# Performance work log

Measured on AMD Instinct MI355X. Metric: run time of the kernel, lower is better.

Reference implementation:

```python
import jax, jax.numpy as jnp
import numpy as np

N_HEADS = 16
LN_EPS = 1e-6


def _mha(q_in, kv_in, mask, wq, bq, wk, bk, wv, bv, wo, bo):
    B, Sq, D = q_in.shape
    H = N_HEADS
    dh = D // H
    def split(x):  # [B,S,D] -> [B,H,S,dh]
        return x.reshape(B, -1, H, dh).transpose(0, 2, 1, 3)
    q = split(q_in @ wq + bq)
    k = split(kv_in @ wk + bk)
    v = split(kv_in @ wv + bv)
    scores = jnp.einsum('bhqd,bhkd->bhqk', q, k) / jnp.sqrt(jnp.asarray(dh, q.dtype))
    scores = scores + mask * (-1e9)
    attn = jax.nn.softmax(scores, axis=-1)
    out = jnp.einsum('bhqk,bhkd->bhqd', attn, v)
    out = out.transpose(0, 2, 1, 3).reshape(B, Sq, D)
    return out @ wo + bo


def _layer_norm(x, gamma, beta):
    mu = jnp.mean(x, axis=-1, keepdims=True)
    var = jnp.mean(jnp.square(x - mu), axis=-1, keepdims=True)
    return (x - mu) * jax.lax.rsqrt(var + LN_EPS) * gamma + beta


def setup_inputs() -> dict:
    key = jax.random.key(0)
    B, S_dec, S_enc, D, F = 4, 1024, 1024, 1024, 4096
    ks = jax.random.split(key, 16)
    s = 0.02
    inp = {
        'inputs': jax.random.normal(ks[0], (B, S_dec, D), jnp.float32),
        'enc_outputs': jax.random.normal(ks[1], (B, S_enc, D), jnp.float32),
        # causal look-ahead mask: 1 above diagonal -> -1e9 added to scores
        'mask_1': jnp.triu(jnp.ones((S_dec, S_dec), jnp.float32), k=1)[None, None],
        'mask_2': jnp.zeros((B, 1, 1, S_enc), jnp.float32),
    }
    names = ['wq1', 'wk1', 'wv1', 'wo1', 'wq2', 'wk2', 'wv2', 'wo2']
    for i, n in enumerate(names):
        inp[n] = jax.random.normal(ks[2 + i], (D, D), jnp.float32) * s
        inp['b' + n[1:]] = jnp.zeros((D,), jnp.float32)
    inp['w_ff1'] = jax.random.normal(ks[10], (D, F), jnp.float32) * s
    inp['b_ff1'] = jnp.zeros((F,), jnp.float32)
    inp['w_ff2'] = jax.random.normal(ks[11], (F, D), jnp.float32) * s
    inp['b_ff2'] = jnp.zeros((D,), jnp.float32)
    for i in (1, 2, 3):
        inp[f'g{i}'] = jnp.ones((D,), jnp.float32)
        inp[f'beta{i}'] = jnp.zeros((D,), jnp.float32)
    return inp


def reference(inputs, enc_outputs, mask_1, mask_2,
              wq1, bq1, wk1, bk1, wv1, bv1, wo1, bo1,
              wq2, bq2, wk2, bk2, wv2, bv2, wo2, bo2,
              w_ff1, b_ff1, w_ff2, b_ff2,
              g1, beta1, g2, beta2, g3, beta3):
    # causal self-attention + residual + LN (dropout inactive at inference)
    attn = _mha(inputs, inputs, mask_1, wq1, bq1, wk1, bk1, wv1, bv1, wo1, bo1)
    attn = _layer_norm(attn + inputs, g1, beta1)
    # encoder-decoder cross-attention + residual + LN
    attn2 = _mha(attn, enc_outputs, mask_2, wq2, bq2, wk2, bk2, wv2, bv2, wo2, bo2)
    attn2 = _layer_norm(attn2 + attn, g2, beta2)
    # FFN + residual + LN
    h = jax.nn.relu(attn2 @ w_ff1 + b_ff1)
    h = h @ w_ff2 + b_ff2
    return _layer_norm(h + attn2, g3, beta3)
```

## Files before the change

kernel.cpp:

```cpp
#include <hip/hip_runtime.h>
#include <stdint.h>

typedef unsigned short ushort_t;
typedef __attribute__((ext_vector_type(8))) short bf16x8;
typedef __attribute__((ext_vector_type(4))) float f32x4;
typedef __attribute__((ext_vector_type(4))) unsigned short us4;

#define DEV __device__ __forceinline__

DEV unsigned short f2bf(float f) {
  union { float f; unsigned u; } x; x.f = f;
  unsigned r = x.u + 0x7fffu + ((x.u >> 16) & 1u);
  return (unsigned short)(r >> 16);
}

DEV void gload16(const void* g, void* l) {
  __builtin_amdgcn_global_load_lds(
      (const __attribute__((address_space(1))) unsigned int*)g,
      (__attribute__((address_space(3))) unsigned int*)l, 16, 0, 0);
}

#define MFMA16 __builtin_amdgcn_mfma_f32_16x16x32_bf16

__global__ __launch_bounds__(256) void cast_bf16_kernel(
    const float* __restrict__ x, ushort_t* __restrict__ y, int n4) {
  int i = blockIdx.x * 256 + threadIdx.x;
  if (i >= n4) return;
  float4 v = ((const float4*)x)[i];
  us4 o; o.x = f2bf(v.x); o.y = f2bf(v.y); o.z = f2bf(v.z); o.w = f2bf(v.w);
  ((us4*)y)[i] = o;
}

__global__ __launch_bounds__(256) void reduce_cast_kernel(
    const float* __restrict__ p0, const float* __restrict__ p1,
    ushort_t* __restrict__ y, int n4) {
  int i = blockIdx.x * 256 + threadIdx.x;
  if (i >= n4) return;
  float4 a = ((const float4*)p0)[i];
  float4 b = ((const float4*)p1)[i];
  us4 o; o.x = f2bf(a.x + b.x); o.y = f2bf(a.y + b.y);
  o.z = f2bf(a.z + b.z); o.w = f2bf(a.w + b.w);
  ((us4*)y)[i] = o;
}

__global__ __launch_bounds__(256) void transpose_cast_kernel(
    const float* __restrict__ W, ushort_t* __restrict__ dst, int K, int N) {
  __shared__ float tile[64][65];
  int n0 = blockIdx.x * 64, k0 = blockIdx.y * 64;
  int tid = threadIdx.x;
#pragma unroll
  for (int it = 0; it < 16; ++it) {
    int idx = it * 256 + tid; int r = idx >> 6, c = idx & 63;
    tile[r][c] = W[(size_t)(k0 + r) * N + n0 + c];
  }
  __syncthreads();
#pragma unroll
  for (int it = 0; it < 16; ++it) {
    int idx = it * 256 + tid; int r = idx >> 6, c = idx & 63;
    dst[(size_t)(n0 + r) * K + k0 + c] = f2bf(tile[c][r]);
  }
}

struct Src8 { const float* p[8]; };
__global__ __launch_bounds__(256) void transpose_cast8_kernel(
    Src8 s, ushort_t* __restrict__ dst) {
  __shared__ float tile[64][65];
  const float* W = s.p[blockIdx.z];
  ushort_t* out = dst + (size_t)blockIdx.z * 1048576;
  int n0 = blockIdx.x * 64, k0 = blockIdx.y * 64;
  int tid = threadIdx.x;
#pragma unroll
  for (int it = 0; it < 16; ++it) {
    int idx = it * 256 + tid; int r = idx >> 6, c = idx & 63;
    tile[r][c] = W[(size_t)(k0 + r) * 1024 + n0 + c];
  }
  __syncthreads();
#pragma unroll
  for (int it = 0; it < 16; ++it) {
    int idx = it * 256 + tid; int r = idx >> 6, c = idx & 63;
    out[(size_t)(n0 + r) * 1024 + k0 + c] = f2bf(tile[c][r]);
  }
}

__global__ __launch_bounds__(256) void transpose_v_kernel(
    const ushort_t* __restrict__ V, int ldv, ushort_t* __restrict__ vT) {
  __shared__ ushort_t tile[64][65];
  int s0 = blockIdx.x * 64;
  int bh = blockIdx.y;
  int b = bh >> 4, h = bh & 15;
  int tid = threadIdx.x;
#pragma unroll
  for (int it = 0; it < 4; ++it) {
    int idx = it * 256 + tid; int r = idx >> 4, c = (idx & 15) * 4;
    us4 v = *(const us4*)&V[(size_t)(b * 1024 + s0 + r) * ldv + h * 64 + c];
    tile[r][c] = v.x; tile[r][c + 1] = v.y; tile[r][c + 2] = v.z; tile[r][c + 3] = v.w;
  }
  __syncthreads();
#pragma unroll
  for (int it = 0; it < 4; ++it) {
    int idx = it * 256 + tid; int r = idx >> 4, c = (idx & 15) * 4;
    us4 o; o.x = tile[c][r]; o.y = tile[c + 1][r]; o.z = tile[c + 2][r]; o.w = tile[c + 3][r];
    *(us4*)&vT[((size_t)bh * 64 + r) * 1024 + s0 + c] = o;
  }
}

template <int WF32, int WB16, int RELU>
__global__ __launch_bounds__(256, 2) void gemm_bt(
    const ushort_t* __restrict__ A, const ushort_t* __restrict__ Bt,
    const float* __restrict__ b0, const float* __restrict__ b1,
    const float* __restrict__ b2, const float* __restrict__ b3,
    float* __restrict__ Cf, ushort_t* __restrict__ Cb,
    int M, int N, int K, int Ks, long long pstr) {
  __shared__ ushort_t sA[4096];
  __shared__ ushort_t sB[4096];
  const int tid = threadIdx.x;
  const int w = tid >> 6, lane = tid & 63;
  const int lrow = lane & 15, lk = lane >> 4;
  const int m0 = blockIdx.x * 128, n0 = blockIdx.y * 128;
  const int kz = blockIdx.z * Ks;
  const int wr = w >> 1, wc = w & 1;
  f32x4 acc[4][4] = {};
  const int brow0 = (w * 1024 + lane * 16) >> 6;
  const int kbyte = (lane * 16) & 63;

  for (int kt = kz; kt < kz + Ks; kt += 32) {
    __syncthreads();
    const ushort_t* ga = A + (size_t)(m0 + brow0) * K + kt + (kbyte >> 1);
    gload16(ga, (char*)sA + w * 1024);
    gload16(ga + (size_t)64 * K, (char*)sA + 4096 + w * 1024);
    const ushort_t* gb = Bt + (size_t)(n0 + brow0) * K + kt + (kbyte >> 1);
    gload16(gb, (char*)sB + w * 1024);
    gload16(gb + (size_t)64 * K, (char*)sB + 4096 + w * 1024);
    __syncthreads();
    bf16x8 aF[4], bF[4];
#pragma unroll
    for (int t = 0; t < 4; ++t) {
      aF[t] = *(const bf16x8*)((const char*)sA + ((wr * 64 + t * 16 + lrow) << 6) + (lk << 4));
      bF[t] = *(const bf16x8*)((const char*)sB + ((wc * 64 + t * 16 + lrow) << 6) + (lk << 4));
    }
#pragma unroll
    for (int mt = 0; mt < 4; ++mt)
#pragma unroll
      for (int nt = 0; nt < 4; ++nt)
        acc[mt][nt] = MFMA16(aF[mt], bF[nt], acc[mt][nt], 0, 0, 0);
  }
  float* Cfz = Cf + (long long)blockIdx.z * pstr;
#pragma unroll
  for (int nt = 0; nt < 4; ++nt) {
    int col = n0 + wc * 64 + nt * 16 + lrow;
    int seg = col >> 10;
    const float* bp = seg == 0 ? b0 : seg == 1 ? b1 : seg == 2 ? b2 : b3;
    float bv = bp[col & 1023];
    if (blockIdx.z != 0) bv = 0.f;
#pragma unroll
    for (int mt = 0; mt < 4; ++mt) {
      int rowb = m0 + wr * 64 + mt * 16 + lk * 4;
#pragma unroll
      for (int j = 0; j < 4; ++j) {
        float v = acc[mt][nt][j] + bv;
        if (RELU) v = fmaxf(v, 0.f);
        size_t idx = (size_t)(rowb + j) * N + col;
        if (WF32) Cfz[idx] = v;
        if (WB16) Cb[idx] = f2bf(v);
      }
    }
  }
}

template <int WF32, int WB16, int RELU>
__global__ __launch_bounds__(512, 1) void gemm256(
    const ushort_t* __restrict__ A, const ushort_t* __restrict__ Bt,
    const float* __restrict__ b0, const float* __restrict__ b1,
    const float* __restrict__ b2, const float* __restrict__ b3,
    float* __restrict__ Cf, ushort_t* __restrict__ Cb,
    int M, int N, int K, int Ks, long long pstr) {
  extern __shared__ char L[];
  const int tid = threadIdx.x;
  const int w = tid >> 6, lane = tid & 63;
  const int lrow = lane & 15, lk = lane >> 4;
  const int wm = w >> 2, wn = w & 3;
  const int m0 = blockIdx.x * 256, n0 = blockIdx.y * 256;
  const int kz = blockIdx.z * Ks;
  const int nt = Ks >> 6;

  const int srow = w * 8 + (lane >> 3);
  const int gsw = (lane & 7) ^ ((lane >> 3) & 7);
  const ushort_t* srcA = A + (size_t)(m0 + srow) * K + kz + gsw * 8;
  const ushort_t* srcB = Bt + (size_t)(n0 + srow) * K + kz + gsw * 8;
  const int dstw = w * 1024;

#define STG(M_, T_)                                                   \
  do {                                                                \
    const ushort_t* g0 = ((M_) ? srcB : srcA) + (size_t)(T_) * 64;    \
    char* d_ = L + (((T_) & 1) << 16) + ((M_) << 15) + dstw;          \
    gload16(g0, d_);                                                  \
    gload16(g0 + (size_t)64 * K, d_ + 8192);                          \
    gload16(g0 + (size_t)128 * K, d_ + 16384);                        \
    gload16(g0 + (size_t)192 * K, d_ + 24576);                        \
  } while (0)

  f32x4 acc[8][4] = {};
  const int swz = (lrow & 7) << 4;
  const int k0b = (lk << 4) ^ swz;
  const int k1b = (64 + (lk << 4)) ^ swz;
  const int aBase = (wm * 128 + lrow) << 7;
  const int bBase = ((wn * 64 + lrow) << 7) + 32768;

  STG(0, 0); STG(1, 0); STG(0, 1);
  asm volatile("s_waitcnt vmcnt(4)" ::: "memory");
  __builtin_amdgcn_s_barrier();

  for (int t = 0; t < nt; ++t) {
    const int buf = (t & 1) << 16;
    const char* base = L + buf;
    bf16x8 aF[8], bF0, bF1;
    {
#pragma unroll
      for (int m = 0; m < 8; ++m) aF[m] = *(const bf16x8*)(base + aBase + m * 2048 + k0b);
      bF0 = *(const bf16x8*)(base + bBase + k0b);
      bF1 = *(const bf16x8*)(base + bBase + 2048 + k0b);
      if (t + 1 < nt) STG(1, t + 1);
      __builtin_amdgcn_s_barrier();
      __builtin_amdgcn_s_setprio(1);
#pragma unroll
      for (int m = 0; m < 8; ++m) {
        acc[m][0] = MFMA16(aF[m], bF0, acc[m][0], 0, 0, 0);
        acc[m][1] = MFMA16(aF[m], bF1, acc[m][1], 0, 0, 0);
      }
      __builtin_amdgcn_s_setprio(0);
      __builtin_amdgcn_s_barrier();
    }
    {
      bF0 = *(const bf16x8*)(base + bBase + 4096 + k0b);
      bF1 = *(const bf16x8*)(base + bBase + 6144 + k0b);
      __builtin_amdgcn_s_barrier();
      __builtin_amdgcn_s_setprio(1);
#pragma unroll
      for (int m = 0; m < 8; ++m) {
        acc[m][2] = MFMA16(aF[m], bF0, acc[m][2], 0, 0, 0);
        acc[m][3] = MFMA16(aF[m], bF1, acc[m][3], 0, 0, 0);
      }
      __builtin_amdgcn_s_setprio(0);
      __builtin_amdgcn_s_barrier();
    }
    {
#pragma unroll
      for (int m = 0; m < 8; ++m) aF[m] = *(const bf16x8*)(base + aBase + m * 2048 + k1b);
      bF0 = *(const bf16x8*)(base + bBase + k1b);
      bF1 = *(const bf16x8*)(base + bBase + 2048 + k1b);
      __builtin_amdgcn_s_barrier();
      __builtin_amdgcn_s_setprio(1);
#pragma unroll
      for (int m = 0; m < 8; ++m) {
        acc[m][0] = MFMA16(aF[m], bF0, acc[m][0], 0, 0, 0);
        acc[m][1] = MFMA16(aF[m], bF1, acc[m][1], 0, 0, 0);
      }
      __builtin_amdgcn_s_setprio(0);
      __builtin_amdgcn_s_barrier();
    }
    {
      bF0 = *(const bf16x8*)(base + bBase + 4096 + k1b);
      bF1 = *(const bf16x8*)(base + bBase + 6144 + k1b);
      if (t + 2 < nt) {
        STG(0, t + 2);
        asm volatile("s_waitcnt vmcnt(4)" ::: "memory");
      } else {
        asm volatile("s_waitcnt vmcnt(0)" ::: "memory");
      }
      __builtin_amdgcn_s_barrier();
      __builtin_amdgcn_s_setprio(1);
#pragma unroll
      for (int m = 0; m < 8; ++m) {
        acc[m][2] = MFMA16(aF[m], bF0, acc[m][2], 0, 0, 0);
        acc[m][3] = MFMA16(aF[m], bF1, acc[m][3], 0, 0, 0);
      }
      __builtin_amdgcn_s_setprio(0);
      __builtin_amdgcn_s_barrier();
    }
  }
#undef STG

  float* Cfz = Cf + (long long)blockIdx.z * pstr;
#pragma unroll
  for (int n = 0; n < 4; ++n) {
    int col = n0 + wn * 64 + n * 16 + lrow;
    int seg = col >> 10;
    const float* bp = seg == 0 ? b0 : seg == 1 ? b1 : seg == 2 ? b2 : b3;
    float bv = bp[col & 1023];
    if (blockIdx.z != 0) bv = 0.f;
#pragma unroll
    for (int m = 0; m < 8; ++m) {
      int rowb = m0 + wm * 128 + m * 16 + lk * 4;
#pragma unroll
      for (int j = 0; j < 4; ++j) {
        float v = acc[m][n][j] + bv;
        if (RELU) v = fmaxf(v, 0.f);
        size_t idx = (size_t)(rowb + j) * N + col;
        if (WF32) Cfz[idx] = v;
        if (WB16) Cb[idx] = f2bf(v);
      }
    }
  }
}

template <int CAUSAL>
__global__ __launch_bounds__(256, 3) void attn_kernel(
    const ushort_t* __restrict__ Q, int ldq,
    const ushort_t* __restrict__ Kp, int ldk,
    const ushort_t* __restrict__ vT,
    const float* __restrict__ mask2,
    ushort_t* __restrict__ O) {
  __shared__ ushort_t sK[2][4096];
  __shared__ ushort_t sV[2][4096];
  __shared__ ushort_t sP[4][2048];
  const int bh = blockIdx.x, qb = blockIdx.y;
  const int b = bh >> 4, h = bh & 15;
  const int tid = threadIdx.x, w = tid >> 6, lane = tid & 63;
  const int lrow = lane & 15, lk = lane >> 4;
  const int q0 = qb * 128 + w * 32;

  bf16x8 qF[2][2];
#pragma unroll
  for (int g = 0; g < 2; ++g) {
    const ushort_t* qptr =
        Q + (size_t)(b * 1024 + q0 + g * 16 + lrow) * ldq + h * 64 + lk * 8;
    qF[g][0] = *(const bf16x8*)qptr;
    qF[g][1] = *(const bf16x8*)(qptr + 32);
  }
  f32x4 oacc[2][4] = {};
  float m_[2] = {-3.0e38f, -3.0e38f}, l_[2] = {0.f, 0.f};
  const int nkb = CAUSAL ? (qb * 2 + 2) : 16;
  const float C = 0.18033688011112042f;

  const int sr = w * 16 + (lane >> 3);
  const int scb = (((lane & 7) ^ (lane >> 3)) * 16);
  const ushort_t* kbase = Kp + (size_t)(b * 1024 + sr) * ldk + h * 64 + (scb >> 1);
  const ushort_t* vbase = vT + ((size_t)bh * 64 + sr) * 1024 + (scb >> 1);
  char* dstK0 = (char*)sK[0] + w * 2048;
  char* dstV0 = (char*)sV[0] + w * 2048;

#define STAGE(kb_, bufi)                                              \
  do {                                                                \
    const ushort_t* gk = kbase + (size_t)(kb_) * 64 * ldk;            \
    gload16(gk, dstK0 + (bufi) * 8192);                               \
    gload16(gk + (size_t)8 * ldk, dstK0 + (bufi) * 8192 + 1024);      \
    const ushort_t* gv = vbase + (kb_) * 64;                          \
    gload16(gv, dstV0 + (bufi) * 8192);                               \
    gload16(gv + (size_t)8 * 1024, dstV0 + (bufi) * 8192 + 1024);     \
  } while (0)

  STAGE(0, 0);
  const int swz = (lrow & 7) << 4;

  for (int kb = 0; kb < nkb; ++kb) {
    const int buf = kb & 1;
    __syncthreads();
    if (kb + 1 < nkb) STAGE(kb + 1, buf ^ 1);

    const char* kB = (const char*)sK[buf];
    const char* vB = (const char*)sV[buf];
    bool skip[2], edge[2];
#pragma unroll
    for (int g = 0; g < 2; ++g) {
      int qming = q0 + g * 16;
      skip[g] = CAUSAL && (kb * 64 > qming + 15);
      edge[g] = CAUSAL && !skip[g] && (kb * 64 + 63 > qming);
    }
    f32x4 sc[2][4];
    __builtin_amdgcn_s_setprio(1);
#pragma unroll
    for (int kt = 0; kt < 4; ++kt) {
      const char* rp = kB + ((kt * 16 + lrow) << 7);
      bf16x8 k0 = *(const bf16x8*)(rp + ((lk * 16) ^ swz));
      bf16x8 k1 = *(const bf16x8*)(rp + ((64 + lk * 16) ^ swz));
      f32x4 z0 = {};
      z0 = MFMA16(k0, qF[0][0], z0, 0, 0, 0);
      sc[0][kt] = MFMA16(k1, qF[0][1], z0, 0, 0, 0);
      f32x4 z1 = {};
      z1 = MFMA16(k0, qF[1][0], z1, 0, 0, 0);
      sc[1][kt] = MFMA16(k1, qF[1][1], z1, 0, 0, 0);
    }
    __builtin_amdgcn_s_setprio(0);
    float4 mv[4];
    if (!CAUSAL) {
#pragma unroll
      for (int kt = 0; kt < 4; ++kt)
        mv[kt] = *(const float4*)&mask2[b * 1024 + kb * 64 + kt * 16 + lk * 4];
    }
#pragma unroll
    for (int g = 0; g < 2; ++g) {
      if (skip[g]) continue;
      if (CAUSAL) {
        if (edge[g]) {
          int qrel = q0 + g * 16 + lrow - kb * 64;
#pragma unroll
          for (int kt = 0; kt < 4; ++kt)
#pragma unroll
            for (int j = 0; j < 4; ++j)
              if (kt * 16 + lk * 4 + j > qrel) sc[g][kt][j] = -3.0e38f;
        }
      } else {
#pragma unroll
        for (int kt = 0; kt < 4; ++kt) {
          sc[g][kt][0] = fmaf(mv[kt].x, -8e9f, sc[g][kt][0]);
          sc[g][kt][1] = fmaf(mv[kt].y, -8e9f, sc[g][kt][1]);
          sc[g][kt][2] = fmaf(mv[kt].z, -8e9f, sc[g][kt][2]);
          sc[g][kt][3] = fmaf(mv[kt].w, -8e9f, sc[g][kt][3]);
        }
      }
      float pmax = fmaxf(
          fmaxf(fmaxf(sc[g][0][0], sc[g][0][1]), fmaxf(sc[g][0][2], sc[g][0][3])),
          fmaxf(fmaxf(sc[g][1][0], sc[g][1][1]), fmaxf(sc[g][1][2], sc[g][1][3])));
      pmax = fmaxf(pmax, fmaxf(
          fmaxf(fmaxf(sc[g][2][0], sc[g][2][1]), fmaxf(sc[g][2][2], sc[g][2][3])),
          fmaxf(fmaxf(sc[g][3][0], sc[g][3][1]), fmaxf(sc[g][3][2], sc[g][3][3]))));
      pmax = fmaxf(pmax, __shfl_xor(pmax, 16));
      pmax = fmaxf(pmax, __shfl_xor(pmax, 32));
      if (__any(pmax - m_[g] > 64.f)) {
        float mnew = fmaxf(m_[g], pmax);
        float scale = __builtin_exp2f((m_[g] - mnew) * C);
        l_[g] *= scale;
        m_[g] = mnew;
#pragma unroll
        for (int j = 0; j < 4; ++j) {
          float sj = __shfl(scale, lk * 4 + j);
          oacc[g][0][j] *= sj; oacc[g][1][j] *= sj;
          oacc[g][2][j] *= sj; oacc[g][3][j] *= sj;
        }
      }
      const float mC = m_[g] * C;
      float ps = 0.f;
#pragma unroll
      for (int kt = 0; kt < 4; ++kt)
#pragma unroll
        for (int j = 0; j < 4; ++j) {
          float e = __builtin_exp2f(fmaf(sc[g][kt][j], C, -mC));
          sc[g][kt][j] = e;
          ps += e;
        }
      ps += __shfl_xor(ps, 16);
      ps += __shfl_xor(ps, 32);
      l_[g] += ps;
      char* bp = (char*)sP[w] + (g * 16 + lrow) * 128;
#pragma unroll
      for (int kt = 0; kt < 4; ++kt) {
        unsigned d0, d1;
        asm("v_cvt_pk_bf16_f32 %0, %1, %2" : "=v"(d0) : "v"(sc[g][kt][0]), "v"(sc[g][kt][1]));
        asm("v_cvt_pk_bf16_f32 %0, %1, %2" : "=v"(d1) : "v"(sc[g][kt][2]), "v"(sc[g][kt][3]));
        uint2 dd; dd.x = d0; dd.y = d1;
        *(uint2*)(bp + ((kt * 32 + lk * 8) ^ swz)) = dd;
      }
    }
    bf16x8 pF[2][2];
#pragma unroll
    for (int g = 0; g < 2; ++g) {
      if (skip[g]) continue;
      const char* pB = (const char*)sP[w] + (g * 16 + lrow) * 128;
      pF[g][0] = *(const bf16x8*)(pB + ((lk * 16) ^ swz));
      pF[g][1] = *(const bf16x8*)(pB + ((64 + lk * 16) ^ swz));
    }
    __builtin_amdgcn_s_setprio(1);
#pragma unroll
    for (int t = 0; t < 4; ++t) {
      const char* rp = vB + ((t * 16 + lrow) << 7);
      bf16x8 v0 = *(const bf16x8*)(rp + ((lk * 16) ^ swz));
      bf16x8 v1 = *(const bf16x8*)(rp + ((64 + lk * 16) ^ swz));
      if (!skip[0]) {
        oacc[0][t] = MFMA16(pF[0][0], v0, oacc[0][t], 0, 0, 0);
        oacc[0][t] = MFMA16(pF[0][1], v1, oacc[0][t], 0, 0, 0);
      }
      if (!skip[1]) {
        oacc[1][t] = MFMA16(pF[1][0], v0, oacc[1][t], 0, 0, 0);
        oacc[1][t] = MFMA16(pF[1][1], v1, oacc[1][t], 0, 0, 0);
      }
    }
    __builtin_amdgcn_s_setprio(0);
  }
#undef STAGE
#pragma unroll
  for (int g = 0; g < 2; ++g)
#pragma unroll
    for (int j = 0; j < 4; ++j) {
      float lj = __shfl(l_[g], lk * 4 + j);
      float invl = 1.f / lj;
      int row = q0 + g * 16 + lk * 4 + j;
      ushort_t* op = O + (size_t)(b * 1024 + row) * 1024 + h * 64;
#pragma unroll
      for (int t = 0; t < 4; ++t) op[t * 16 + lrow] = f2bf(oacc[g][t][j] * invl);
    }
}

template <int WB16, int NPART>
__global__ __launch_bounds__(256) void ln_kernel(
    const float* __restrict__ p0, const float* __restrict__ p1,
    const float* __restrict__ p2, const float* __restrict__ p3,
    const float* __restrict__ r,
    const float* __restrict__ g, const float* __restrict__ be,
    float* __restrict__ yf, ushort_t* __restrict__ yb) {
  int row = blockIdx.x, tid = threadIdx.x;
  size_t off = (size_t)row * 1024;
  float4 va = ((const float4*)(p0 + off))[tid];
  if (NPART >= 2) {
    float4 t = ((const float4*)(p1 + off))[tid];
    va.x += t.x; va.y += t.y; va.z += t.z; va.w += t.w;
  }
  if (NPART >= 4) {
    float4 t2 = ((const float4*)(p2 + off))[tid];
    float4 t3 = ((const float4*)(p3 + off))[tid];
    va.x += t2.x + t3.x; va.y += t2.y + t3.y;
    va.z += t2.z + t3.z; va.w += t2.w + t3.w;
  }
  float4 vb = ((const float4*)(r + off))[tid];
  float x0 = va.x + vb.x, x1 = va.y + vb.y, x2 = va.z + vb.z, x3 = va.w + vb.w;
  float s = x0 + x1 + x2 + x3;
  float s2 = x0 * x0 + x1 * x1 + x2 * x2 + x3 * x3;
#pragma unroll
  for (int o = 1; o < 64; o <<= 1) { s += __shfl_xor(s, o); s2 += __shfl_xor(s2, o); }
  __shared__ float sh[8];
  if ((tid & 63) == 0) { sh[tid >> 6] = s; sh[4 + (tid >> 6)] = s2; }
  __syncthreads();
  s = sh[0] + sh[1] + sh[2] + sh[3];
  s2 = sh[4] + sh[5] + sh[6] + sh[7];
  float mu = s * 0.0009765625f;
  float var = s2 * 0.0009765625f - mu * mu;
  float inv = rsqrtf(var + 1e-6f);
  float4 gv = ((const float4*)g)[tid];
  float4 bv = ((const float4*)be)[tid];
  float y0 = (x0 - mu) * inv * gv.x + bv.x;
  float y1 = (x1 - mu) * inv * gv.y + bv.y;
  float y2 = (x2 - mu) * inv * gv.z + bv.z;
  float y3 = (x3 - mu) * inv * gv.w + bv.w;
  ((float4*)(yf + off))[tid] = make_float4(y0, y1, y2, y3);
  if (WB16) {
    us4 o; o.x = f2bf(y0); o.y = f2bf(y1); o.z = f2bf(y2); o.w = f2bf(y3);
    ((us4*)(yb + off))[tid] = o;
  }
}

extern "C" void kernel_launch(void* const* d_in, const int* in_sizes, int n_in,
                              void* d_out, int out_size, void* d_ws, size_t ws_size,
                              hipStream_t stream) {
  (void)in_sizes; (void)n_in; (void)out_size; (void)ws_size;
  const float* inputs = (const float*)d_in[0];
  const float* enc    = (const float*)d_in[1];
  const float* mask2  = (const float*)d_in[3];
  const float* wq1 = (const float*)d_in[4];  const float* bq1 = (const float*)d_in[5];
  const float* wk1 = (const float*)d_in[6];  const float* bk1 = (const float*)d_in[7];
  const float* wv1 = (const float*)d_in[8];  const float* bv1 = (const float*)d_in[9];
  const float* wo1 = (const float*)d_in[10]; const float* bo1 = (const float*)d_in[11];
  const float* wq2 = (const float*)d_in[12]; const float* bq2 = (const float*)d_in[13];
  const float* wk2 = (const float*)d_in[14]; const float* bk2 = (const float*)d_in[15];
  const float* wv2 = (const float*)d_in[16]; const float* bv2 = (const float*)d_in[17];
  const float* wo2 = (const float*)d_in[18]; const float* bo2 = (const float*)d_in[19];
  const float* wff1 = (const float*)d_in[20]; const float* bff1 = (const float*)d_in[21];
  const float* wff2 = (const float*)d_in[22]; const float* bff2 = (const float*)d_in[23];
  const float* g1 = (const float*)d_in[24]; const float* be1 = (const float*)d_in[25];
  const float* g2 = (const float*)d_in[26]; const float* be2 = (const float*)d_in[27];
  const float* g3 = (const float*)d_in[28]; const float* be3 = (const float*)d_in[29];

  char* ws = (char*)d_ws;
  const size_t MB = 1024 * 1024;
  const size_t W1M = 1048576;
  ushort_t* wt    = (ushort_t*)ws;
  ushort_t* xb    = (ushort_t*)(ws + 32 * MB);
  ushort_t* encb  = (ushort_t*)(ws + 40 * MB);
  ushort_t* qkvb  = (ushort_t*)(ws + 48 * MB);
  ushort_t* vtb   = (ushort_t*)(ws + 72 * MB);
  ushort_t* attnb = (ushort_t*)(ws + 80 * MB);
  ushort_t* y1b   = (ushort_t*)(ws + 88 * MB);
  ushort_t* y2b   = (ushort_t*)(ws + 96 * MB);
  float*    c1f   = (float*)(ws + 104 * MB);
  float*    p48f  = (float*)(ws + 48 * MB);
  float*    y1f   = (float*)(ws + 120 * MB);
  float*    y2f   = (float*)(ws + 136 * MB);
  ushort_t* q2b   = (ushort_t*)(ws + 32 * MB);
  ushort_t* kv2b  = (ushort_t*)(ws + 56 * MB);
  ushort_t* hb    = (ushort_t*)(ws + 32 * MB);
  float*    pff   = (float*)(ws + 72 * MB);
  float* outf = (float*)d_out;
  const long long PELEMS = 4 * 1024 * 1024;
  const long long P48OFF = (long long)(p48f - c1f);

  cast_bf16_kernel<<<4096, 256, 0, stream>>>(inputs, xb, 1048576);
  cast_bf16_kernel<<<4096, 256, 0, stream>>>(enc, encb, 1048576);
  Src8 s8; s8.p[0] = wq1; s8.p[1] = wk1; s8.p[2] = wv1; s8.p[3] = wo1;
           s8.p[4] = wq2; s8.p[5] = wk2; s8.p[6] = wv2; s8.p[7] = wo2;
  transpose_cast8_kernel<<<dim3(16, 16, 8), 256, 0, stream>>>(s8, wt);
  transpose_cast_kernel<<<dim3(64, 16), 256, 0, stream>>>(wff1, wt + 8 * W1M, 1024, 4096);
  transpose_cast_kernel<<<dim3(16, 64), 256, 0, stream>>>(wff2, wt + 12 * W1M, 4096, 1024);

  gemm256<0, 1, 0><<<dim3(16, 12, 1), 512, 131072, stream>>>(
      xb, wt, bq1, bk1, bv1, bv1, nullptr, qkvb, 4096, 3072, 1024, 1024, 0);
  transpose_v_kernel<<<dim3(16, 64), 256, 0, stream>>>(qkvb + 2048, 3072, vtb);
  attn_kernel<1><<<dim3(64, 8), 256, 0, stream>>>(
      qkvb, 3072, qkvb + 1024, 3072, vtb, nullptr, attnb);
  gemm_bt<1, 0, 0><<<dim3(32, 8, 2), 256, 0, stream>>>(
      attnb, wt + 3 * W1M, bo1, bo1, bo1, bo1, c1f, nullptr, 4096, 1024, 1024, 512, P48OFF);
  ln_kernel<1, 2><<<4096, 256, 0, stream>>>(c1f, p48f, nullptr, nullptr,
                                            inputs, g1, be1, y1f, y1b);

  gemm_bt<1, 0, 0><<<dim3(32, 8, 2), 256, 0, stream>>>(
      y1b, wt + 4 * W1M, bq2, bq2, bq2, bq2, c1f, nullptr, 4096, 1024, 1024, 512, P48OFF);
  reduce_cast_kernel<<<4096, 256, 0, stream>>>(c1f, p48f, q2b, 1048576);
  gemm_bt<0, 1, 0><<<dim3(32, 16, 1), 256, 0, stream>>>(
      encb, wt + 5 * W1M, bk2, bv2, bk2, bk2, nullptr, kv2b, 4096, 2048, 1024, 1024, 0);
  transpose_v_kernel<<<dim3(16, 64), 256, 0, stream>>>(kv2b + 1024, 2048, vtb);
  attn_kernel<0><<<dim3(64, 8), 256, 0, stream>>>(
      q2b, 1024, kv2b, 2048, vtb, mask2, attnb);
  gemm_bt<1, 0, 0><<<dim3(32, 8, 2), 256, 0, stream>>>(
      attnb, wt + 7 * W1M, bo2, bo2, bo2, bo2, c1f, nullptr, 4096, 1024, 1024, 512, P48OFF);
  ln_kernel<1, 2><<<4096, 256, 0, stream>>>(c1f, p48f, nullptr, nullptr,
                                            y1f, g2, be2, y2f, y2b);

  gemm256<0, 1, 1><<<dim3(16, 16, 1), 512, 131072, stream>>>(
      y2b, wt + 8 * W1M, bff1, bff1 + 1024, bff1 + 2048, bff1 + 3072,
      nullptr, hb, 4096, 4096, 1024, 1024, 0);
  gemm256<1, 0, 0><<<dim3(16, 4, 4), 512, 131072, stream>>>(
      hb, wt + 12 * W1M, bff2, bff2, bff2, bff2, pff, nullptr,
      4096, 1024, 4096, 1024, PELEMS);
  ln_kernel<0, 4><<<4096, 256, 0, stream>>>(pff, pff + PELEMS, pff + 2 * PELEMS,
                                            pff + 3 * PELEMS, y2f, g3, be3, outf, nullptr);
}
```

Before: 372.4 us.

## Store split-K partials and residuals in bf16 and split GEMM staging loads

Split-K GEMM partial outputs are now written in bf16 rather than fp32. The LayerNorm and reduce kernels read those bf16 partials and also take bf16 residuals in place of fp32 copies, so the fp32 y1/y2 activations are no longer written. Separately, the gemm256 prefetch is split into half-tile stages interleaved across the k-substeps, and the LDS fragment read order is changed. This cuts memory traffic, at the cost of more rounding error in residuals and partial sums.

```diff
diff --git a/kernel.cpp b/kernel.cpp
--- a/kernel.cpp
+++ b/kernel.cpp
@@ -12,6 +12,10 @@
   union { float f; unsigned u; } x; x.f = f;
   unsigned r = x.u + 0x7fffu + ((x.u >> 16) & 1u);
   return (unsigned short)(r >> 16);
+}
+
+DEV float bf2f(unsigned short u) {
+  union { unsigned u; float f; } x; x.u = (unsigned)u << 16; return x.f;
 }
 
 DEV void gload16(const void* g, void* l) {
@@ -32,14 +36,17 @@
 }
 
 __global__ __launch_bounds__(256) void reduce_cast_kernel(
-    const float* __restrict__ p0, const float* __restrict__ p1,
+    const ushort_t* __restrict__ p0, const ushort_t* __restrict__ p1,
     ushort_t* __restrict__ y, int n4) {
   int i = blockIdx.x * 256 + threadIdx.x;
   if (i >= n4) return;
-  float4 a = ((const float4*)p0)[i];
-  float4 b = ((const float4*)p1)[i];
-  us4 o; o.x = f2bf(a.x + b.x); o.y = f2bf(a.y + b.y);
-  o.z = f2bf(a.z + b.z); o.w = f2bf(a.w + b.w);
+  us4 a = ((const us4*)p0)[i];
+  us4 b = ((const us4*)p1)[i];
+  us4 o;
+  o.x = f2bf(bf2f(a.x) + bf2f(b.x));
+  o.y = f2bf(bf2f(a.y) + bf2f(b.y));
+  o.z = f2bf(bf2f(a.z) + bf2f(b.z));
+  o.w = f2bf(bf2f(a.w) + bf2f(b.w));
   ((us4*)y)[i] = o;
 }
 
@@ -104,13 +111,12 @@
   }
 }
 
-template <int WF32, int WB16, int RELU>
+template <int RELU>
 __global__ __launch_bounds__(256, 2) void gemm_bt(
     const ushort_t* __restrict__ A, const ushort_t* __restrict__ Bt,
     const float* __restrict__ b0, const float* __restrict__ b1,
     const float* __restrict__ b2, const float* __restrict__ b3,
-    float* __restrict__ Cf, ushort_t* __restrict__ Cb,
-    int M, int N, int K, int Ks, long long pstr) {
+    ushort_t* __restrict__ Cb, int M, int N, int K, int Ks, long long pstr) {
   __shared__ ushort_t sA[4096];
   __shared__ ushort_t sB[4096];
   const int tid = threadIdx.x;
@@ -135,8 +141,8 @@
     bf16x8 aF[4], bF[4];
 #pragma unroll
     for (int t = 0; t < 4; ++t) {
+      bF[t] = *(const bf16x8*)((const char*)sB + ((wc * 64 + t * 16 + lrow) << 6) + (lk << 4));
       aF[t] = *(const bf16x8*)((const char*)sA + ((wr * 64 + t * 16 + lrow) << 6) + (lk << 4));
-      bF[t] = *(const bf16x8*)((const char*)sB + ((wc * 64 + t * 16 + lrow) << 6) + (lk << 4));
     }
 #pragma unroll
     for (int mt = 0; mt < 4; ++mt)
@@ -144,7 +150,7 @@
       for (int nt = 0; nt < 4; ++nt)
         acc[mt][nt] = MFMA16(aF[mt], bF[nt], acc[mt][nt], 0, 0, 0);
   }
-  float* Cfz = Cf + (long long)blockIdx.z * pstr;
+  ushort_t* Cbz = Cb + (long long)blockIdx.z * pstr;
 #pragma unroll
   for (int nt = 0; nt < 4; ++nt) {
     int col = n0 + wc * 64 + nt * 16 + lrow;
@@ -159,21 +165,18 @@
       for (int j = 0; j < 4; ++j) {
         float v = acc[mt][nt][j] + bv;
         if (RELU) v = fmaxf(v, 0.f);
-        size_t idx = (size_t)(rowb + j) * N + col;
-        if (WF32) Cfz[idx] = v;
-        if (WB16) Cb[idx] = f2bf(v);
-      }
-    }
-  }
-}
-
-template <int WF32, int WB16, int RELU>
+        Cbz[(size_t)(rowb + j) * N + col] = f2bf(v);
+      }
+    }
+  }
+}
+
+template <int RELU>
 __global__ __launch_bounds__(512, 1) void gemm256(
     const ushort_t* __restrict__ A, const ushort_t* __restrict__ Bt,
     const float* __restrict__ b0, const float* __restrict__ b1,
     const float* __restrict__ b2, const float* __restrict__ b3,
-    float* __restrict__ Cf, ushort_t* __restrict__ Cb,
-    int M, int N, int K, int Ks, long long pstr) {
+    ushort_t* __restrict__ Cb, int M, int N, int K, int Ks, long long pstr) {
   extern __shared__ char L[];
   const int tid = threadIdx.x;
   const int w = tid >> 6, lane = tid & 63;
@@ -189,14 +192,13 @@
   const ushort_t* srcB = Bt + (size_t)(n0 + srow) * K + kz + gsw * 8;
   const int dstw = w * 1024;
 
-#define STG(M_, T_)                                                   \
-  do {                                                                \
-    const ushort_t* g0 = ((M_) ? srcB : srcA) + (size_t)(T_) * 64;    \
-    char* d_ = L + (((T_) & 1) << 16) + ((M_) << 15) + dstw;          \
-    gload16(g0, d_);                                                  \
-    gload16(g0 + (size_t)64 * K, d_ + 8192);                          \
-    gload16(g0 + (size_t)128 * K, d_ + 16384);                        \
-    gload16(g0 + (size_t)192 * K, d_ + 24576);                        \
+#define STG2(M_, T_, S_)                                                     \
+  do {                                                                       \
+    const ushort_t* g0 = ((M_) ? srcB : srcA) + (size_t)(T_) * 64 +          \
+                         (size_t)(S_) * 64 * K;                              \
+    char* d_ = L + (((T_) & 1) << 16) + ((M_) << 15) + (S_) * 8192 + dstw;   \
+    gload16(g0, d_);                                                         \
+    gload16(g0 + (size_t)64 * K, d_ + 8192);                                 \
   } while (0)
 
   f32x4 acc[8][4] = {};
@@ -206,7 +208,8 @@
   const int aBase = (wm * 128 + lrow) << 7;
   const int bBase = ((wn * 64 + lrow) << 7) + 32768;
 
-  STG(0, 0); STG(1, 0); STG(0, 1);
+  STG2(0, 0, 0); STG2(0, 0, 2); STG2(1, 0, 0); STG2(1, 0, 2);
+  STG2(0, 1, 0); STG2(0, 1, 2);
   asm volatile("s_waitcnt vmcnt(4)" ::: "memory");
   __builtin_amdgcn_s_barrier();
 
@@ -215,11 +218,11 @@
     const char* base = L + buf;
     bf16x8 aF[8], bF0, bF1;
     {
-#pragma unroll
-      for (int m = 0; m < 8; ++m) aF[m] = *(const bf16x8*)(base + aBase + m * 2048 + k0b);
       bF0 = *(const bf16x8*)(base + bBase + k0b);
       bF1 = *(const bf16x8*)(base + bBase + 2048 + k0b);
-      if (t + 1 < nt) STG(1, t + 1);
+#pragma unroll
+      for (int m = 0; m < 8; ++m) aF[m] = *(const bf16x8*)(base + aBase + m * 2048 + k0b);
+      if (t + 1 < nt) STG2(1, t + 1, 0);
       __builtin_amdgcn_s_barrier();
       __builtin_amdgcn_s_setprio(1);
 #pragma unroll
@@ -233,6 +236,7 @@
     {
       bF0 = *(const bf16x8*)(base + bBase + 4096 + k0b);
       bF1 = *(const bf16x8*)(base + bBase + 6144 + k0b);
+      if (t + 1 < nt) STG2(1, t + 1, 2);
       __builtin_amdgcn_s_barrier();
       __builtin_amdgcn_s_setprio(1);
 #pragma unroll
@@ -244,10 +248,10 @@
       __builtin_amdgcn_s_barrier();
     }
     {
-#pragma unroll
-      for (int m = 0; m < 8; ++m) aF[m] = *(const bf16x8*)(base + aBase + m * 2048 + k1b);
       bF0 = *(const bf16x8*)(base + bBase + k1b);
       bF1 = *(const bf16x8*)(base + bBase + 2048 + k1b);
+#pragma unroll
+      for (int m = 0; m < 8; ++m) aF[m] = *(const bf16x8*)(base + aBase + m * 2048 + k1b);
       __builtin_amdgcn_s_barrier();
       __builtin_amdgcn_s_setprio(1);
 #pragma unroll
@@ -262,7 +266,7 @@
       bF0 = *(const bf16x8*)(base + bBase + 4096 + k1b);
       bF1 = *(const bf16x8*)(base + bBase + 6144 + k1b);
       if (t + 2 < nt) {
-        STG(0, t + 2);
+        STG2(0, t + 2, 0); STG2(0, t + 2, 2);
         asm volatile("s_waitcnt vmcnt(4)" ::: "memory");
       } else {
         asm volatile("s_waitcnt vmcnt(0)" ::: "memory");
@@ -278,9 +282,9 @@
       __builtin_amdgcn_s_barrier();
     }
   }
-#undef STG
-
-  float* Cfz = Cf + (long long)blockIdx.z * pstr;
+#undef STG2
+
+  ushort_t* Cbz = Cb + (long long)blockIdx.z * pstr;
 #pragma unroll
   for (int n = 0; n < 4; ++n) {
     int col = n0 + wn * 64 + n * 16 + lrow;
@@ -295,9 +299,7 @@
       for (int j = 0; j < 4; ++j) {
         float v = acc[m][n][j] + bv;
         if (RELU) v = fmaxf(v, 0.f);
-        size_t idx = (size_t)(rowb + j) * N + col;
-        if (WF32) Cfz[idx] = v;
-        if (WB16) Cb[idx] = f2bf(v);
+        Cbz[(size_t)(rowb + j) * N + col] = f2bf(v);
       }
     }
   }
@@ -490,28 +492,34 @@
     }
 }
 
-template <int WB16, int NPART>
+template <int RESBF, int NPART, int WF32>
 __global__ __launch_bounds__(256) void ln_kernel(
-    const float* __restrict__ p0, const float* __restrict__ p1,
-    const float* __restrict__ p2, const float* __restrict__ p3,
-    const float* __restrict__ r,
+    const ushort_t* __restrict__ p0, const ushort_t* __restrict__ p1,
+    const ushort_t* __restrict__ p2, const ushort_t* __restrict__ p3,
+    const void* __restrict__ rp,
     const float* __restrict__ g, const float* __restrict__ be,
     float* __restrict__ yf, ushort_t* __restrict__ yb) {
   int row = blockIdx.x, tid = threadIdx.x;
-  size_t off = (size_t)row * 1024;
-  float4 va = ((const float4*)(p0 + off))[tid];
+  size_t off = (size_t)row * 1024 + tid * 4;
+  us4 a = *(const us4*)(p0 + off);
+  float x0 = bf2f(a.x), x1 = bf2f(a.y), x2 = bf2f(a.z), x3 = bf2f(a.w);
   if (NPART >= 2) {
-    float4 t = ((const float4*)(p1 + off))[tid];
-    va.x += t.x; va.y += t.y; va.z += t.z; va.w += t.w;
+    us4 t = *(const us4*)(p1 + off);
+    x0 += bf2f(t.x); x1 += bf2f(t.y); x2 += bf2f(t.z); x3 += bf2f(t.w);
   }
   if (NPART >= 4) {
-    float4 t2 = ((const float4*)(p2 + off))[tid];
-    float4 t3 = ((const float4*)(p3 + off))[tid];
-    va.x += t2.x + t3.x; va.y += t2.y + t3.y;
-    va.z += t2.z + t3.z; va.w += t2.w + t3.w;
-  }
-  float4 vb = ((const float4*)(r + off))[tid];
-  float x0 = va.x + vb.x, x1 = va.y + vb.y, x2 = va.z + vb.z, x3 = va.w + vb.w;
+    us4 t2 = *(const us4*)(p2 + off);
+    us4 t3 = *(const us4*)(p3 + off);
+    x0 += bf2f(t2.x) + bf2f(t3.x); x1 += bf2f(t2.y) + bf2f(t3.y);
+    x2 += bf2f(t2.z) + bf2f(t3.z); x3 += bf2f(t2.w) + bf2f(t3.w);
+  }
+  if (RESBF) {
+    us4 r = *(const us4*)((const ushort_t*)rp + off);
+    x0 += bf2f(r.x); x1 += bf2f(r.y); x2 += bf2f(r.z); x3 += bf2f(r.w);
+  } else {
+    float4 r = *(const float4*)((const float*)rp + off);
+    x0 += r.x; x1 += r.y; x2 += r.z; x3 += r.w;
+  }
   float s = x0 + x1 + x2 + x3;
   float s2 = x0 * x0 + x1 * x1 + x2 * x2 + x3 * x3;
 #pragma unroll
@@ -524,16 +532,17 @@
   float mu = s * 0.0009765625f;
   float var = s2 * 0.0009765625f - mu * mu;
   float inv = rsqrtf(var + 1e-6f);
-  float4 gv = ((const float4*)g)[tid];
-  float4 bv = ((const float4*)be)[tid];
+  float4 gv = *(const float4*)(g + tid * 4);
+  float4 bv = *(const float4*)(be + tid * 4);
   float y0 = (x0 - mu) * inv * gv.x + bv.x;
   float y1 = (x1 - mu) * inv * gv.y + bv.y;
   float y2 = (x2 - mu) * inv * gv.z + bv.z;
   float y3 = (x3 - mu) * inv * gv.w + bv.w;
-  ((float4*)(yf + off))[tid] = make_float4(y0, y1, y2, y3);
-  if (WB16) {
+  if (WF32) {
+    *(float4*)(yf + off) = make_float4(y0, y1, y2, y3);
+  } else {
     us4 o; o.x = f2bf(y0); o.y = f2bf(y1); o.z = f2bf(y2); o.w = f2bf(y3);
-    ((us4*)(yb + off))[tid] = o;
+    *(us4*)(yb + off) = o;
   }
 }
 
@@ -569,17 +578,13 @@
   ushort_t* attnb = (ushort_t*)(ws + 80 * MB);
   ushort_t* y1b   = (ushort_t*)(ws + 88 * MB);
   ushort_t* y2b   = (ushort_t*)(ws + 96 * MB);
-  float*    c1f   = (float*)(ws + 104 * MB);
-  float*    p48f  = (float*)(ws + 48 * MB);
-  float*    y1f   = (float*)(ws + 120 * MB);
-  float*    y2f   = (float*)(ws + 136 * MB);
+  ushort_t* cp    = (ushort_t*)(ws + 104 * MB);
   ushort_t* q2b   = (ushort_t*)(ws + 32 * MB);
   ushort_t* kv2b  = (ushort_t*)(ws + 56 * MB);
   ushort_t* hb    = (ushort_t*)(ws + 32 * MB);
-  float*    pff   = (float*)(ws + 72 * MB);
+  ushort_t* pp    = (ushort_t*)(ws + 104 * MB);
   float* outf = (float*)d_out;
-  const long long PELEMS = 4 * 1024 * 1024;
-  const long long P48OFF = (long long)(p48f - c1f);
+  const long long PE = 4LL * 1024 * 1024;
 
   cast_bf16_kernel<<<4096, 256, 0, stream>>>(inputs, xb, 1048576);
   cast_bf16_kernel<<<4096, 256, 0, stream>>>(enc, encb, 1048576);
@@ -589,35 +594,34 @@
   transpose_cast_kernel<<<dim3(64, 16), 256, 0, stream>>>(wff1, wt + 8 * W1M, 1024, 4096);
   transpose_cast_kernel<<<dim3(16, 64), 256, 0, stream>>>(wff2, wt + 12 * W1M, 4096, 1024);
 
-  gemm256<0, 1, 0><<<dim3(16, 12, 1), 512, 131072, stream>>>(
-      xb, wt, bq1, bk1, bv1, bv1, nullptr, qkvb, 4096, 3072, 1024, 1024, 0);
+  gemm256<0><<<dim3(16, 12, 1), 512, 131072, stream>>>(
+      xb, wt, bq1, bk1, bv1, bv1, qkvb, 4096, 3072, 1024, 1024, 0);
   transpose_v_kernel<<<dim3(16, 64), 256, 0, stream>>>(qkvb + 2048, 3072, vtb);
   attn_kernel<1><<<dim3(64, 8), 256, 0, stream>>>(
       qkvb, 3072, qkvb + 1024, 3072, vtb, nullptr, attnb);
-  gemm_bt<1, 0, 0><<<dim3(32, 8, 2), 256, 0, stream>>>(
-      attnb, wt + 3 * W1M, bo1, bo1, bo1, bo1, c1f, nullptr, 4096, 1024, 1024, 512, P48OFF);
-  ln_kernel<1, 2><<<4096, 256, 0, stream>>>(c1f, p48f, nullptr, nullptr,
-                                            inputs, g1, be1, y1f, y1b);
-
-  gemm_bt<1, 0, 0><<<dim3(32, 8, 2), 256, 0, stream>>>(
-      y1b, wt + 4 * W1M, bq2, bq2, bq2, bq2, c1f, nullptr, 4096, 1024, 1024, 512, P48OFF);
-  reduce_cast_kernel<<<4096, 256, 0, stream>>>(c1f, p48f, q2b, 1048576);
-  gemm_bt<0, 1, 0><<<dim3(32, 16, 1), 256, 0, stream>>>(
-      encb, wt + 5 * W1M, bk2, bv2, bk2, bk2, nullptr, kv2b, 4096, 2048, 1024, 1024, 0);
+  gemm_bt<0><<<dim3(32, 8, 2), 256, 0, stream>>>(
+      attnb, wt + 3 * W1M, bo1, bo1, bo1, bo1, cp, 4096, 1024, 1024, 512, PE);
+  ln_kernel<0, 2, 0><<<4096, 256, 0, stream>>>(cp, cp + PE, nullptr, nullptr,
+                                               inputs, g1, be1, nullptr, y1b);
+
+  gemm_bt<0><<<dim3(32, 8, 2), 256, 0, stream>>>(
+      y1b, wt + 4 * W1M, bq2, bq2, bq2, bq2, cp, 4096, 1024, 1024, 512, PE);
+  reduce_cast_kernel<<<4096, 256, 0, stream>>>(cp, cp + PE, q2b, 1048576);
+  gemm_bt<0><<<dim3(32, 16, 1), 256, 0, stream>>>(
+      encb, wt + 5 * W1M, bk2, bv2, bk2, bk2, kv2b, 4096, 2048, 1024, 1024, 0);
   transpose_v_kernel<<<dim3(16, 64), 256, 0, stream>>>(kv2b + 1024, 2048, vtb);
   attn_kernel<0><<<dim3(64, 8), 256, 0, stream>>>(
       q2b, 1024, kv2b, 2048, vtb, mask2, attnb);
-  gemm_bt<1, 0, 0><<<dim3(32, 8, 2), 256, 0, stream>>>(
-      attnb, wt + 7 * W1M, bo2, bo2, bo2, bo2, c1f, nullptr, 4096, 1024, 1024, 512, P48OFF);
-  ln_kernel<1, 2><<<4096, 256, 0, stream>>>(c1f, p48f, nullptr, nullptr,
-                                            y1f, g2, be2, y2f, y2b);
-
-  gemm256<0, 1, 1><<<dim3(16, 16, 1), 512, 131072, stream>>>(
+  gemm_bt<0><<<dim3(32, 8, 2), 256, 0, stream>>>(
+      attnb, wt + 7 * W1M, bo2, bo2, bo2, bo2, cp, 4096, 1024, 1024, 512, PE);
+  ln_kernel<1, 2, 0><<<4096, 256, 0, stream>>>(cp, cp + PE, nullptr, nullptr,
+                                               y1b, g2, be2, nullptr, y2b);
+
+  gemm256<1><<<dim3(16, 16, 1), 512, 131072, stream>>>(
       y2b, wt + 8 * W1M, bff1, bff1 + 1024, bff1 + 2048, bff1 + 3072,
-      nullptr, hb, 4096, 4096, 1024, 1024, 0);
-  gemm256<1, 0, 0><<<dim3(16, 4, 4), 512, 131072, stream>>>(
-      hb, wt + 12 * W1M, bff2, bff2, bff2, bff2, pff, nullptr,
-      4096, 1024, 4096, 1024, PELEMS);
-  ln_kernel<0, 4><<<4096, 256, 0, stream>>>(pff, pff + PELEMS, pff + 2 * PELEMS,
-                                            pff + 3 * PELEMS, y2f, g3, be3, outf, nullptr);
-}
+      hb, 4096, 4096, 1024, 1024, 0);
+  gemm256<0><<<dim3(16, 4, 4), 512, 131072, stream>>>(
+      hb, wt + 12 * W1M, bff2, bff2, bff2, bff2, pp, 4096, 1024, 4096, 1024, PE);
+  ln_kernel<1, 4, 1><<<4096, 256, 0, stream>>>(pp, pp + PE, pp + 2 * PE, pp + 3 * PE,
+                                               y2b, g3, be3, outf, nullptr);
+}
```

New measurement: 353.9 us. 1.05x faster.
